# Kernel tuning notes

Measured on AMD Instinct MI355X. Metric: run time of the kernel, lower is better.

The kernel has to match this reference:

```python
import jax, jax.numpy as jnp
import numpy as np

B, N_IN, D_IN = 64, 2048, 16
N_OUT, D_OUT = 32, 32
ROUTINGS = 3
EPS = 1e-7


def squash(s, axis=-1):
    # standard CapsNet squash: s * ||s||^2 / (1 + ||s||^2) / ||s||
    sq_norm = jnp.sum(jnp.square(s), axis=axis, keepdims=True)
    scale = sq_norm / (1.0 + sq_norm) / jnp.sqrt(sq_norm + EPS)
    return s * scale


def setup_inputs() -> dict:
    key = jax.random.key(0)
    k1, k2 = jax.random.split(key)
    inputs = jax.random.normal(k1, (B, N_IN, D_IN), dtype=jnp.float32)
    # glorot-uniform-ish scale for [N_out, N_in, D_out, D_in] weight
    limit = np.sqrt(6.0 / (D_IN + D_OUT)).astype(np.float32)
    weight_matrix = jax.random.uniform(k2, (N_OUT, N_IN, D_OUT, D_IN), dtype=jnp.float32,
                                       minval=-limit, maxval=limit)
    return {"inputs": inputs, "weight_matrix": weight_matrix}


def reference(inputs, weight_matrix):
    # u_hat[b,o,i,d] = W[o,i,d,k] @ x[b,i,k]  (replaces tile + map_fn matmul)
    u_hat = jnp.einsum('oidk,bik->boid', weight_matrix, inputs)  # [B, N_out, N_in, D_out]
    b_logits = jnp.zeros((inputs.shape[0], N_OUT, 1, N_IN), dtype=u_hat.dtype)
    v = None
    for r in range(ROUTINGS):
        c = jax.nn.softmax(b_logits, axis=1)                      # softmax over output capsules
        s = jnp.einsum('boli,boid->bold', c, u_hat)               # [B, N_out, 1, D_out]
        v = squash(s)
        if r < ROUTINGS - 1:
            b_logits = b_logits + jnp.einsum('bold,boid->boli', v, u_hat)
    return jnp.squeeze(v, axis=2)                                 # [B, N_out, D_out]
```

## Files before the change

### kernel.cpp

```cpp
#include <hip/hip_runtime.h>

#define B_    64
#define NI    2048
#define DK    16
#define NO    32
#define DOUT  32
#define EPSQ  1e-7f

typedef unsigned u32x2 __attribute__((ext_vector_type(2)));
typedef unsigned u32x4 __attribute__((ext_vector_type(4)));

__device__ __forceinline__ unsigned pack2_bf16(float a, float b) {
    unsigned ua = __float_as_uint(a);
    unsigned ub = __float_as_uint(b);
    ua = (ua + 0x7fffu + ((ua >> 16) & 1u)) >> 16;
    ub = (ub + 0x7fffu + ((ub >> 16) & 1u)) >> 16;
    return ua | (ub << 16);
}
__device__ __forceinline__ float bf_lo(unsigned w) { return __uint_as_float(w << 16); }
__device__ __forceinline__ float bf_hi(unsigned w) { return __uint_as_float(w & 0xffff0000u); }


constexpr int WSTRIDE = 516;

__global__ __launch_bounds__(512)
void compute_uhat(const float* __restrict__ x, const float* __restrict__ W,
                  ushort* __restrict__ U)
{
    __shared__ float Ws[NO * WSTRIDE];
    __shared__ float xs[B_ * DK];
    const int i = blockIdx.x;
    const int t = threadIdx.x;

    if (t < 256) {
        const int b = t >> 2, k4 = t & 3;
        float4 v = *(const float4*)(x + ((size_t)b * NI + i) * DK + k4 * 4);
        *(float4*)&xs[b * DK + k4 * 4] = v;
    }

    #pragma unroll
    for (int jj = 0; jj < 8; ++jj) {
        const int p  = t + 512 * jj;
        const int oo = p >> 7;
        const int cc = p & 127;
        float4 v = ((const float4*)(W + ((size_t)oo * NI + i) * (DOUT * DK)))[cc];
        *(float4*)&Ws[oo * WSTRIDE + cc * 4] = v;
    }

    const int o  = t & 31;
    const int q  = (t >> 5) & 7;
    const int bh = t >> 8;

    __syncthreads();

    float w[64];
    {
        const float* wr = &Ws[o * WSTRIDE + q * 64];
        #pragma unroll
        for (int m = 0; m < 16; ++m) {
            float4 v = *(const float4*)(wr + 4 * m);
            w[4*m+0] = v.x; w[4*m+1] = v.y; w[4*m+2] = v.z; w[4*m+3] = v.w;
        }
    }

    const int j = q >> 1, half = q & 1;

    for (int bb = 0; bb < 32; ++bb) {
        const int b = bh * 32 + bb;
        const float4* xv = (const float4*)&xs[b * DK];
        const float4 x0 = xv[0], x1 = xv[1], x2 = xv[2], x3 = xv[3];

        float acc[4];
        #pragma unroll
        for (int dl = 0; dl < 4; ++dl) {
            const float* wr = &w[dl * 16];
            float a;
            a  = wr[0]  * x0.x + wr[1]  * x0.y + wr[2]  * x0.z + wr[3]  * x0.w;
            a += wr[4]  * x1.x + wr[5]  * x1.y + wr[6]  * x1.z + wr[7]  * x1.w;
            a += wr[8]  * x2.x + wr[9]  * x2.y + wr[10] * x2.z + wr[11] * x2.w;
            a += wr[12] * x3.x + wr[13] * x3.y + wr[14] * x3.z + wr[15] * x3.w;
            acc[dl] = a;
        }

        u32x2 pk;
        pk.x = pack2_bf16(acc[0], acc[1]);
        pk.y = pack2_bf16(acc[2], acc[3]);
        const size_t off = ((((size_t)b * NI + i) * 4 + j) * NO + o) * 8 + half * 4;
        __builtin_nontemporal_store(pk, (u32x2*)(U + off));
    }
}

constexpr int SU_SEG = 16;
constexpr int SU_IPB = NI / SU_SEG;

__global__ __launch_bounds__(256)
void sum_u(const ushort* __restrict__ U, float* __restrict__ s0)
{
    const int t    = threadIdx.x;
    const int b    = blockIdx.x >> 4;
    const int iseg = blockIdx.x & (SU_SEG - 1);
    const int c    = t & 127;
    const int half = t >> 7;

    float acc[8];
    #pragma unroll
    for (int k = 0; k < 8; ++k) acc[k] = 0.f;

    const u32x4* up = (const u32x4*)U
        + ((size_t)b * NI + (size_t)iseg * SU_IPB + half) * 128 + c;

    #pragma unroll 8
    for (int it = 0; it < SU_IPB / 2; ++it) {
        u32x4 w = __builtin_nontemporal_load(up);
        up += 256;
        acc[0] += bf_lo(w.x); acc[1] += bf_hi(w.x);
        acc[2] += bf_lo(w.y); acc[3] += bf_hi(w.y);
        acc[4] += bf_lo(w.z); acc[5] += bf_hi(w.z);
        acc[6] += bf_lo(w.w); acc[7] += bf_hi(w.w);
    }

    const int o = c & 31, j = c >> 5;
    float* sp = s0 + (size_t)b * (NO * DOUT) + o * DOUT + j * 8;
    #pragma unroll
    for (int k = 0; k < 8; ++k)
        atomicAdd(&sp[k], acc[k] * 0.03125f);
}

__device__ __forceinline__ void proc_one(const u32x4* cr, const float* vs, float* sacc)
{
    unsigned cw[16];
    #pragma unroll
    for (int jj = 0; jj < 4; ++jj) {
        cw[4*jj+0] = cr[jj].x; cw[4*jj+1] = cr[jj].y;
        cw[4*jj+2] = cr[jj].z; cw[4*jj+3] = cr[jj].w;
    }

    float l0 = 0.f, l1 = 0.f, l2 = 0.f, l3 = 0.f;
    #pragma unroll
    for (int m = 0; m < 16; m += 4) {
        const int d0 = (m >> 2) * 8;
        l0 = fmaf(vs[d0+0], bf_lo(cw[m+0]), l0);
        l0 = fmaf(vs[d0+1], bf_hi(cw[m+0]), l0);
        l1 = fmaf(vs[d0+2], bf_lo(cw[m+1]), l1);
        l1 = fmaf(vs[d0+3], bf_hi(cw[m+1]), l1);
        l2 = fmaf(vs[d0+4], bf_lo(cw[m+2]), l2);
        l2 = fmaf(vs[d0+5], bf_hi(cw[m+2]), l2);
        l3 = fmaf(vs[d0+6], bf_lo(cw[m+3]), l3);
        l3 = fmaf(vs[d0+7], bf_hi(cw[m+3]), l3);
    }
    const float logit = (l0 + l1) + (l2 + l3);

    float mx = logit;
    #pragma unroll
    for (int msk = 16; msk >= 1; msk >>= 1) mx = fmaxf(mx, __shfl_xor(mx, msk));
    const float e = __expf(logit - mx);
    float ssum = e;
    #pragma unroll
    for (int msk = 16; msk >= 1; msk >>= 1) ssum += __shfl_xor(ssum, msk);
    const float c = e / ssum;

    #pragma unroll
    for (int m = 0; m < 16; ++m) {
        const int d0 = (m >> 2) * 8 + (m & 3) * 2;
        sacc[d0]     = fmaf(c, bf_lo(cw[m]), sacc[d0]);
        sacc[d0 + 1] = fmaf(c, bf_hi(cw[m]), sacc[d0 + 1]);
    }
}

constexpr int BPB = 16;
constexpr int NIB = NI / BPB / 16;

template<int R>
__global__ __launch_bounds__(256)
void routing_mid(const ushort* __restrict__ U, const float* __restrict__ sA,
                 const float* __restrict__ sB, float* __restrict__ s_out)
{
    __shared__ float sblk[NO * DOUT];
    __shared__ float vsh[NO][DOUT + 1];
    const int t  = threadIdx.x;
    const int b  = blockIdx.x >> 4;
    const int i0 = (blockIdx.x & (BPB - 1)) * (NI / BPB);

    {
        const int oo = t >> 3;
        const int dg = t & 7;
        float4 sv = *(const float4*)(sA + ((size_t)b * NO + oo) * DOUT + dg * 4);
        float sq = sv.x*sv.x + sv.y*sv.y + sv.z*sv.z + sv.w*sv.w;
        #pragma unroll
        for (int msk = 4; msk >= 1; msk >>= 1) sq += __shfl_xor(sq, msk);
        float sc = sq / (1.f + sq) * rsqrtf(sq + EPSQ);
        float v0 = sv.x * sc, v1 = sv.y * sc, v2 = sv.z * sc, v3 = sv.w * sc;
        if (R == 2) {
            float4 s2v = *(const float4*)(sB + ((size_t)b * NO + oo) * DOUT + dg * 4);
            float sq2 = s2v.x*s2v.x + s2v.y*s2v.y + s2v.z*s2v.z + s2v.w*s2v.w;
            #pragma unroll
            for (int msk = 4; msk >= 1; msk >>= 1) sq2 += __shfl_xor(sq2, msk);
            float sc2 = sq2 / (1.f + sq2) * rsqrtf(sq2 + EPSQ);
            v0 += s2v.x * sc2; v1 += s2v.y * sc2; v2 += s2v.z * sc2; v3 += s2v.w * sc2;
        }
        vsh[oo][dg*4+0] = v0; vsh[oo][dg*4+1] = v1;
        vsh[oo][dg*4+2] = v2; vsh[oo][dg*4+3] = v3;
    }
    for (int n = t; n < NO * DOUT; n += 256) sblk[n] = 0.f;
    __syncthreads();

    const int o  = t & 31;
    const int hw = t >> 5;

    float vs[DOUT];
    #pragma unroll
    for (int d = 0; d < DOUT; ++d) vs[d] = vsh[o][d];

    float sacc[DOUT];
    #pragma unroll
    for (int d = 0; d < DOUT; ++d) sacc[d] = 0.f;

    const u32x4* up = (const u32x4*)U + ((size_t)b * NI + i0 + 2 * hw) * (4 * NO) + o;
    const size_t step = (size_t)16 * 4 * NO;

    u32x4 cur[8];
    #pragma unroll
    for (int jj = 0; jj < 4; ++jj) {
        cur[jj]     = __builtin_nontemporal_load(up + jj * NO);
        cur[4 + jj] = __builtin_nontemporal_load(up + 4 * NO + jj * NO);
    }
    up += step;

    for (int ii = 0; ii < NIB; ++ii) {
        u32x4 nxt[8];
        if (ii + 1 < NIB) {
            #pragma unroll
            for (int jj = 0; jj < 4; ++jj) {
                nxt[jj]     = __builtin_nontemporal_load(up + jj * NO);
                nxt[4 + jj] = __builtin_nontemporal_load(up + 4 * NO + jj * NO);
            }
            up += step;
        }

        proc_one(&cur[0], vs, sacc);
        proc_one(&cur[4], vs, sacc);

        #pragma unroll
        for (int jj = 0; jj < 8; ++jj) cur[jj] = nxt[jj];
    }

    #pragma unroll
    for (int d = 0; d < DOUT; ++d) sacc[d] += __shfl_xor(sacc[d], 32);

    if ((t & 32) == 0) {
        #pragma unroll
        for (int d = 0; d < DOUT; ++d)
            atomicAdd(&sblk[o * DOUT + ((d + o) & 31)], sacc[d]);
    }
    __syncthreads();

    float* sp = s_out + (size_t)b * NO * DOUT;
    for (int n = t; n < NO * DOUT; n += 256) {
        const int oo = n >> 5, ds = n & 31;
        const int dd = (ds - oo) & 31;
        atomicAdd(&sp[oo * DOUT + dd], sblk[n]);
    }
}

__global__ __launch_bounds__(256)
void squash_final(const float* __restrict__ s, float* __restrict__ out)
{
    const int tid  = threadIdx.x;
    const int pair = blockIdx.x * 8 + (tid >> 5);
    const int d    = tid & 31;
    const int idx  = pair * DOUT + d;

    const float val = s[idx];
    float sq = val * val;
    #pragma unroll
    for (int msk = 16; msk >= 1; msk >>= 1) sq += __shfl_xor(sq, msk);

    const float scale = sq / (1.f + sq) * rsqrtf(sq + EPSQ);
    out[idx] = val * scale;
}

__global__ __launch_bounds__(256)
void squash_update(const float* __restrict__ s, float* __restrict__ Vsum,
                   float* __restrict__ out, int last)
{
    const int tid  = threadIdx.x;
    const int pair = blockIdx.x * 8 + (tid >> 5);
    const int d    = tid & 31;
    const int idx  = pair * DOUT + d;

    const float val = s[idx];
    float sq = val * val;
    #pragma unroll
    for (int msk = 16; msk >= 1; msk >>= 1) sq += __shfl_xor(sq, msk);

    const float scale = sq / (1.f + sq) * rsqrtf(sq + EPSQ);
    const float v = val * scale;

    if (last) out[idx] = v;
    else      Vsum[idx] += v;
}

constexpr int BTILE  = 16;
constexpr int ITILE  = 32;
constexpr int CHUNKS = NI / ITILE;
constexpr int GB     = B_ / BTILE;
constexpr int WROW   = DOUT * DK + 4;

__global__ __launch_bounds__(512)
void routing_pass(const float* __restrict__ x, const float* __restrict__ W,
                  const float* __restrict__ Vsum, float* __restrict__ s_out)
{
    __shared__ float W_s[NO * WROW];
    const int tid   = threadIdx.x;
    const int o     = tid & 31;
    const int bl    = tid >> 5;
    const int chunk = blockIdx.x & (CHUNKS - 1);
    const int gb    = blockIdx.x / CHUNKS;
    const int b     = gb * BTILE + bl;

    float vs[DOUT];
    {
        const float4* vp = (const float4*)(Vsum + (size_t)(b * NO + o) * DOUT);
        #pragma unroll
        for (int qq = 0; qq < 8; ++qq) {
            float4 t2 = vp[qq];
            vs[4*qq+0] = t2.x; vs[4*qq+1] = t2.y; vs[4*qq+2] = t2.z; vs[4*qq+3] = t2.w;
        }
    }
    float sacc[DOUT];
    #pragma unroll
    for (int d = 0; d < DOUT; ++d) sacc[d] = 0.f;

    const int o_ld = tid >> 4;
    const int lpos = tid & 15;

    for (int ii = 0; ii < ITILE; ++ii) {
        const int i = chunk * ITILE + ii;
        __syncthreads();
        const float4* wsrc = (const float4*)W + ((size_t)o_ld * NI + i) * (DOUT * DK / 4);
        #pragma unroll
        for (int jj = 0; jj < 8; ++jj) {
            const int f4pos = lpos + 16 * jj;
            float4 v = wsrc[f4pos];
            *(float4*)&W_s[o_ld * WROW + f4pos * 4] = v;
        }
        __syncthreads();

        const float4* xg = (const float4*)(x + ((size_t)b * NI + i) * DK);
        const float4 xr0 = xg[0], xr1 = xg[1], xr2 = xg[2], xr3 = xg[3];

        float u[DOUT];
        float logit = 0.f;
        const float* wrow = &W_s[o * WROW];
        #pragma unroll
        for (int d = 0; d < DOUT; ++d) {
            const float4 w0 = *(const float4*)(wrow + d * DK + 0);
            const float4 w1 = *(const float4*)(wrow + d * DK + 4);
            const float4 w2 = *(const float4*)(wrow + d * DK + 8);
            const float4 w3 = *(const float4*)(wrow + d * DK + 12);
            float acc;
            acc  = w0.x * xr0.x + w0.y * xr0.y + w0.z * xr0.z + w0.w * xr0.w;
            acc += w1.x * xr1.x + w1.y * xr1.y + w1.z * xr1.z + w1.w * xr1.w;
            acc += w2.x * xr2.x + w2.y * xr2.y + w2.z * xr2.z + w2.w * xr2.w;
            acc += w3.x * xr3.x + w3.y * xr3.y + w3.z * xr3.z + w3.w * xr3.w;
            u[d]  = acc;
            logit = fmaf(vs[d], acc, logit);
        }

        float m = logit;
        #pragma unroll
        for (int msk = 16; msk >= 1; msk >>= 1) m = fmaxf(m, __shfl_xor(m, msk));
        const float e = __expf(logit - m);
        float ssum = e;
        #pragma unroll
        for (int msk = 16; msk >= 1; msk >>= 1) ssum += __shfl_xor(ssum, msk);
        const float c = e / ssum;

        #pragma unroll
        for (int d = 0; d < DOUT; ++d) sacc[d] = fmaf(c, u[d], sacc[d]);
    }

    float* sp = s_out + (size_t)(b * NO + o) * DOUT;
    #pragma unroll
    for (int d = 0; d < DOUT; ++d) atomicAdd(&sp[d], sacc[d]);
}

extern "C" void kernel_launch(void* const* d_in, const int* in_sizes, int n_in,
                              void* d_out, int out_size, void* d_ws, size_t ws_size,
                              hipStream_t stream)
{
    const float* x = (const float*)d_in[0];
    const float* W = (const float*)d_in[1];
    float* out = (float*)d_out;

    float* s0 = (float*)d_ws;
    float* s1 = s0 + (size_t)B_ * NO * DOUT;
    float* s2 = s1 + (size_t)B_ * NO * DOUT;
    ushort* U = (ushort*)((char*)d_ws + (1 << 20));

    const size_t need = (1 << 20) + (size_t)B_ * NI * NO * DOUT * sizeof(ushort);

    hipMemsetAsync(d_ws, 0, (size_t)3 * B_ * NO * DOUT * sizeof(float), stream);

    if (ws_size >= need) {
        compute_uhat<<<dim3(NI), dim3(512), 0, stream>>>(x, W, U);
        sum_u<<<dim3(B_ * SU_SEG), dim3(256), 0, stream>>>(U, s0);
        routing_mid<1><<<dim3(B_ * BPB), dim3(256), 0, stream>>>(U, s0, s0, s1);
        routing_mid<2><<<dim3(B_ * BPB), dim3(256), 0, stream>>>(U, s0, s1, s2);
        squash_final<<<dim3(B_ * NO / 8), dim3(256), 0, stream>>>(s2, out);
    } else {
        for (int r = 0; r < 3; ++r) {
            if (r > 0)
                hipMemsetAsync(s0, 0, (size_t)B_ * NO * DOUT * sizeof(float), stream);
            routing_pass<<<dim3(GB * CHUNKS), dim3(512), 0, stream>>>(x, W, s1, s0);
            squash_update<<<dim3(B_ * NO / 8), dim3(256), 0, stream>>>(s0, s1, out, r == 2);
        }
    }
}
```

Before: 470.9 us.

## Split u_hat blocks by output half, use per-segment partial sums instead of atomics

```diff
diff --git a/kernel.cpp b/kernel.cpp
--- a/kernel.cpp
+++ b/kernel.cpp
@@ -10,6 +10,8 @@
 typedef unsigned u32x2 __attribute__((ext_vector_type(2)));
 typedef unsigned u32x4 __attribute__((ext_vector_type(4)));
 
+constexpr int PSEG = 32;
+
 __device__ __forceinline__ unsigned pack2_bf16(float a, float b) {
     unsigned ua = __float_as_uint(a);
     unsigned ub = __float_as_uint(b);
@@ -21,16 +23,18 @@
 __device__ __forceinline__ float bf_hi(unsigned w) { return __uint_as_float(w & 0xffff0000u); }
 
 
-constexpr int WSTRIDE = 516;
-
-__global__ __launch_bounds__(512)
+constexpr int CU_STR = 516;
+
+__global__ __launch_bounds__(512, 8)
 void compute_uhat(const float* __restrict__ x, const float* __restrict__ W,
                   ushort* __restrict__ U)
 {
-    __shared__ float Ws[NO * WSTRIDE];
+    __shared__ float Ws[16 * CU_STR];
     __shared__ float xs[B_ * DK];
-    const int i = blockIdx.x;
-    const int t = threadIdx.x;
+    const int bx = blockIdx.x;
+    const int i  = bx >> 1;
+    const int oh = bx & 1;
+    const int t  = threadIdx.x;
 
     if (t < 256) {
         const int b = t >> 2, k4 = t & 3;
@@ -39,66 +43,74 @@
     }
 
     #pragma unroll
-    for (int jj = 0; jj < 8; ++jj) {
-        const int p  = t + 512 * jj;
+    for (int pp = 0; pp < 4; ++pp) {
+        const int p  = t + 512 * pp;
         const int oo = p >> 7;
         const int cc = p & 127;
-        float4 v = ((const float4*)(W + ((size_t)oo * NI + i) * (DOUT * DK)))[cc];
-        *(float4*)&Ws[oo * WSTRIDE + cc * 4] = v;
-    }
-
-    const int o  = t & 31;
-    const int q  = (t >> 5) & 7;
-    const int bh = t >> 8;
+        float4 v = ((const float4*)(W + ((size_t)(oh * 16 + oo) * NI + i) * (DOUT * DK)))[cc];
+        *(float4*)&Ws[oo * CU_STR + cc * 4] = v;
+    }
+
+    const int o2 = t & 15;
+    const int q  = (t >> 4) & 7;
+    const int bh = t >> 7;
 
     __syncthreads();
 
-    float w[64];
-    {
-        const float* wr = &Ws[o * WSTRIDE + q * 64];
-        #pragma unroll
-        for (int m = 0; m < 16; ++m) {
-            float4 v = *(const float4*)(wr + 4 * m);
-            w[4*m+0] = v.x; w[4*m+1] = v.y; w[4*m+2] = v.z; w[4*m+3] = v.w;
-        }
-    }
-
     const int j = q >> 1, half = q & 1;
-
-    for (int bb = 0; bb < 32; ++bb) {
-        const int b = bh * 32 + bb;
-        const float4* xv = (const float4*)&xs[b * DK];
-        const float4 x0 = xv[0], x1 = xv[1], x2 = xv[2], x3 = xv[3];
-
-        float acc[4];
-        #pragma unroll
-        for (int dl = 0; dl < 4; ++dl) {
-            const float* wr = &w[dl * 16];
-            float a;
-            a  = wr[0]  * x0.x + wr[1]  * x0.y + wr[2]  * x0.z + wr[3]  * x0.w;
-            a += wr[4]  * x1.x + wr[5]  * x1.y + wr[6]  * x1.z + wr[7]  * x1.w;
-            a += wr[8]  * x2.x + wr[9]  * x2.y + wr[10] * x2.z + wr[11] * x2.w;
-            a += wr[12] * x3.x + wr[13] * x3.y + wr[14] * x3.z + wr[15] * x3.w;
-            acc[dl] = a;
-        }
-
-        u32x2 pk;
-        pk.x = pack2_bf16(acc[0], acc[1]);
-        pk.y = pack2_bf16(acc[2], acc[3]);
-        const size_t off = ((((size_t)b * NI + i) * 4 + j) * NO + o) * 8 + half * 4;
-        __builtin_nontemporal_store(pk, (u32x2*)(U + off));
-    }
-}
-
-constexpr int SU_SEG = 16;
-constexpr int SU_IPB = NI / SU_SEG;
-
+    const int o = oh * 16 + o2;
+    const float* wrow = &Ws[o2 * CU_STR + q * 64];
+
+    #pragma unroll
+    for (int bg = 0; bg < 4; ++bg) {
+        const int b0 = bh * 16 + bg * 4;
+        float acc[4][4];
+        #pragma unroll
+        for (int bv = 0; bv < 4; ++bv)
+            #pragma unroll
+            for (int dl = 0; dl < 4; ++dl) acc[bv][dl] = 0.f;
+
+        #pragma unroll
+        for (int k4 = 0; k4 < 4; ++k4) {
+            float4 xr[4];
+            #pragma unroll
+            for (int bv = 0; bv < 4; ++bv)
+                xr[bv] = *(const float4*)&xs[(b0 + bv) * DK + k4 * 4];
+            #pragma unroll
+            for (int dl = 0; dl < 4; ++dl) {
+                const float4 w4 = *(const float4*)&wrow[16 * dl + 4 * k4];
+                #pragma unroll
+                for (int bv = 0; bv < 4; ++bv) {
+                    float a = acc[bv][dl];
+                    a = fmaf(w4.x, xr[bv].x, a);
+                    a = fmaf(w4.y, xr[bv].y, a);
+                    a = fmaf(w4.z, xr[bv].z, a);
+                    a = fmaf(w4.w, xr[bv].w, a);
+                    acc[bv][dl] = a;
+                }
+            }
+        }
+
+        #pragma unroll
+        for (int bv = 0; bv < 4; ++bv) {
+            const int b = b0 + bv;
+            u32x2 pk;
+            pk.x = pack2_bf16(acc[bv][0], acc[bv][1]);
+            pk.y = pack2_bf16(acc[bv][2], acc[bv][3]);
+            const size_t off = ((((size_t)b * NI + i) * 4 + j) * NO + o) * 8 + half * 4;
+            __builtin_nontemporal_store(pk, (u32x2*)(U + off));
+        }
+    }
+}
+
+template<bool PART>
 __global__ __launch_bounds__(256)
 void sum_u(const ushort* __restrict__ U, float* __restrict__ s0)
 {
+    __shared__ float red[128 * 9];
     const int t    = threadIdx.x;
-    const int b    = blockIdx.x >> 4;
-    const int iseg = blockIdx.x & (SU_SEG - 1);
+    const int b    = blockIdx.x >> 5;
+    const int iseg = blockIdx.x & 31;
     const int c    = t & 127;
     const int half = t >> 7;
 
@@ -107,10 +119,10 @@
     for (int k = 0; k < 8; ++k) acc[k] = 0.f;
 
     const u32x4* up = (const u32x4*)U
-        + ((size_t)b * NI + (size_t)iseg * SU_IPB + half) * 128 + c;
+        + ((size_t)b * NI + (size_t)iseg * (NI / PSEG) + half) * 128 + c;
 
     #pragma unroll 8
-    for (int it = 0; it < SU_IPB / 2; ++it) {
+    for (int it = 0; it < (NI / PSEG) / 2; ++it) {
         u32x4 w = __builtin_nontemporal_load(up);
         up += 256;
         acc[0] += bf_lo(w.x); acc[1] += bf_hi(w.x);
@@ -119,185 +131,186 @@
         acc[6] += bf_lo(w.w); acc[7] += bf_hi(w.w);
     }
 
-    const int o = c & 31, j = c >> 5;
-    float* sp = s0 + (size_t)b * (NO * DOUT) + o * DOUT + j * 8;
-    #pragma unroll
-    for (int k = 0; k < 8; ++k)
-        atomicAdd(&sp[k], acc[k] * 0.03125f);
-}
-
-__device__ __forceinline__ void proc_one(const u32x4* cr, const float* vs, float* sacc)
-{
-    unsigned cw[16];
-    #pragma unroll
-    for (int jj = 0; jj < 4; ++jj) {
-        cw[4*jj+0] = cr[jj].x; cw[4*jj+1] = cr[jj].y;
-        cw[4*jj+2] = cr[jj].z; cw[4*jj+3] = cr[jj].w;
-    }
-
-    float l0 = 0.f, l1 = 0.f, l2 = 0.f, l3 = 0.f;
-    #pragma unroll
-    for (int m = 0; m < 16; m += 4) {
-        const int d0 = (m >> 2) * 8;
-        l0 = fmaf(vs[d0+0], bf_lo(cw[m+0]), l0);
-        l0 = fmaf(vs[d0+1], bf_hi(cw[m+0]), l0);
-        l1 = fmaf(vs[d0+2], bf_lo(cw[m+1]), l1);
-        l1 = fmaf(vs[d0+3], bf_hi(cw[m+1]), l1);
-        l2 = fmaf(vs[d0+4], bf_lo(cw[m+2]), l2);
-        l2 = fmaf(vs[d0+5], bf_hi(cw[m+2]), l2);
-        l3 = fmaf(vs[d0+6], bf_lo(cw[m+3]), l3);
-        l3 = fmaf(vs[d0+7], bf_hi(cw[m+3]), l3);
-    }
-    const float logit = (l0 + l1) + (l2 + l3);
-
-    float mx = logit;
-    #pragma unroll
-    for (int msk = 16; msk >= 1; msk >>= 1) mx = fmaxf(mx, __shfl_xor(mx, msk));
-    const float e = __expf(logit - mx);
-    float ssum = e;
-    #pragma unroll
-    for (int msk = 16; msk >= 1; msk >>= 1) ssum += __shfl_xor(ssum, msk);
-    const float c = e / ssum;
-
-    #pragma unroll
-    for (int m = 0; m < 16; ++m) {
-        const int d0 = (m >> 2) * 8 + (m & 3) * 2;
-        sacc[d0]     = fmaf(c, bf_lo(cw[m]), sacc[d0]);
-        sacc[d0 + 1] = fmaf(c, bf_hi(cw[m]), sacc[d0 + 1]);
-    }
-}
-
-constexpr int BPB = 16;
-constexpr int NIB = NI / BPB / 16;
-
-template<int R>
-__global__ __launch_bounds__(256)
+    if (half == 1) {
+        #pragma unroll
+        for (int k = 0; k < 8; ++k) red[c * 9 + k] = acc[k];
+    }
+    __syncthreads();
+    if (half == 0) {
+        #pragma unroll
+        for (int k = 0; k < 8; ++k) acc[k] = (acc[k] + red[c * 9 + k]) * 0.03125f;
+
+        const int o = c & 31, j = c >> 5;
+        if (PART) {
+            float* sp = s0 + ((size_t)(b * PSEG + iseg)) * 1024 + o * 32 + j * 8;
+            float4 lo = {acc[0], acc[1], acc[2], acc[3]};
+            float4 hi = {acc[4], acc[5], acc[6], acc[7]};
+            *(float4*)sp = lo;
+            *(float4*)(sp + 4) = hi;
+        } else {
+            float* sp = s0 + (size_t)b * 1024 + o * 32 + j * 8;
+            #pragma unroll
+            for (int k = 0; k < 8; ++k) atomicAdd(&sp[k], acc[k]);
+        }
+    }
+}
+
+template<int R, bool PART>
+__global__ __launch_bounds__(256, 5)
 void routing_mid(const ushort* __restrict__ U, const float* __restrict__ sA,
                  const float* __restrict__ sB, float* __restrict__ s_out)
 {
     __shared__ float sblk[NO * DOUT];
     __shared__ float vsh[NO][DOUT + 1];
-    const int t  = threadIdx.x;
-    const int b  = blockIdx.x >> 4;
-    const int i0 = (blockIdx.x & (BPB - 1)) * (NI / BPB);
+    const int t    = threadIdx.x;
+    const int b    = blockIdx.x >> 5;
+    const int iseg = blockIdx.x & 31;
+    const int i0   = iseg * (NI / PSEG);
 
     {
         const int oo = t >> 3;
         const int dg = t & 7;
-        float4 sv = *(const float4*)(sA + ((size_t)b * NO + oo) * DOUT + dg * 4);
+        float4 sv;
+        if (PART) {
+            float4 a = {0.f, 0.f, 0.f, 0.f};
+            for (int is = 0; is < PSEG; ++is) {
+                float4 p = *(const float4*)(sA + ((size_t)(b * PSEG + is)) * 1024 + oo * 32 + dg * 4);
+                a.x += p.x; a.y += p.y; a.z += p.z; a.w += p.w;
+            }
+            sv = a;
+        } else {
+            sv = *(const float4*)(sA + (size_t)b * 1024 + oo * 32 + dg * 4);
+        }
         float sq = sv.x*sv.x + sv.y*sv.y + sv.z*sv.z + sv.w*sv.w;
         #pragma unroll
         for (int msk = 4; msk >= 1; msk >>= 1) sq += __shfl_xor(sq, msk);
         float sc = sq / (1.f + sq) * rsqrtf(sq + EPSQ);
         float v0 = sv.x * sc, v1 = sv.y * sc, v2 = sv.z * sc, v3 = sv.w * sc;
         if (R == 2) {
-            float4 s2v = *(const float4*)(sB + ((size_t)b * NO + oo) * DOUT + dg * 4);
+            float4 s2v;
+            if (PART) {
+                float4 a = {0.f, 0.f, 0.f, 0.f};
+                for (int is = 0; is < PSEG; ++is) {
+                    float4 p = *(const float4*)(sB + ((size_t)(b * PSEG + is)) * 1024 + oo * 32 + dg * 4);
+                    a.x += p.x; a.y += p.y; a.z += p.z; a.w += p.w;
+                }
+                s2v = a;
+            } else {
+                s2v = *(const float4*)(sB + (size_t)b * 1024 + oo * 32 + dg * 4);
+            }
             float sq2 = s2v.x*s2v.x + s2v.y*s2v.y + s2v.z*s2v.z + s2v.w*s2v.w;
             #pragma unroll
             for (int msk = 4; msk >= 1; msk >>= 1) sq2 += __shfl_xor(sq2, msk);
             float sc2 = sq2 / (1.f + sq2) * rsqrtf(sq2 + EPSQ);
             v0 += s2v.x * sc2; v1 += s2v.y * sc2; v2 += s2v.z * sc2; v3 += s2v.w * sc2;
         }
-        vsh[oo][dg*4+0] = v0; vsh[oo][dg*4+1] = v1;
-        vsh[oo][dg*4+2] = v2; vsh[oo][dg*4+3] = v3;
+        vsh[oo][dg * 4 + 0] = v0; vsh[oo][dg * 4 + 1] = v1;
+        vsh[oo][dg * 4 + 2] = v2; vsh[oo][dg * 4 + 3] = v3;
     }
     for (int n = t; n < NO * DOUT; n += 256) sblk[n] = 0.f;
     __syncthreads();
 
-    const int o  = t & 31;
-    const int hw = t >> 5;
-
-    float vs[DOUT];
-    #pragma unroll
-    for (int d = 0; d < DOUT; ++d) vs[d] = vsh[o][d];
-
-    float sacc[DOUT];
-    #pragma unroll
-    for (int d = 0; d < DOUT; ++d) sacc[d] = 0.f;
-
-    const u32x4* up = (const u32x4*)U + ((size_t)b * NI + i0 + 2 * hw) * (4 * NO) + o;
-    const size_t step = (size_t)16 * 4 * NO;
-
-    u32x4 cur[8];
-    #pragma unroll
-    for (int jj = 0; jj < 4; ++jj) {
-        cur[jj]     = __builtin_nontemporal_load(up + jj * NO);
-        cur[4 + jj] = __builtin_nontemporal_load(up + 4 * NO + jj * NO);
-    }
-    up += step;
-
-    for (int ii = 0; ii < NIB; ++ii) {
-        u32x4 nxt[8];
-        if (ii + 1 < NIB) {
-            #pragma unroll
-            for (int jj = 0; jj < 4; ++jj) {
-                nxt[jj]     = __builtin_nontemporal_load(up + jj * NO);
-                nxt[4 + jj] = __builtin_nontemporal_load(up + 4 * NO + jj * NO);
-            }
-            up += step;
-        }
-
-        proc_one(&cur[0], vs, sacc);
-        proc_one(&cur[4], vs, sacc);
-
-        #pragma unroll
-        for (int jj = 0; jj < 8; ++jj) cur[jj] = nxt[jj];
-    }
-
-    #pragma unroll
-    for (int d = 0; d < DOUT; ++d) sacc[d] += __shfl_xor(sacc[d], 32);
-
-    if ((t & 32) == 0) {
-        #pragma unroll
-        for (int d = 0; d < DOUT; ++d)
-            atomicAdd(&sblk[o * DOUT + ((d + o) & 31)], sacc[d]);
+    const int lane = t & 63;
+    const int o    = lane & 31;
+    const int dh   = lane >> 5;
+    const int wv   = t >> 6;
+
+    float vs[16];
+    #pragma unroll
+    for (int ld = 0; ld < 16; ++ld) vs[ld] = vsh[o][dh * 16 + ld];
+
+    float sacc[16];
+    #pragma unroll
+    for (int ld = 0; ld < 16; ++ld) sacc[ld] = 0.f;
+
+    const u32x4* up = (const u32x4*)U
+        + (((size_t)b * NI + i0 + wv * 16) * 4 + 2 * dh) * NO + o;
+
+    u32x4 c0 = __builtin_nontemporal_load(up);
+    u32x4 c1 = __builtin_nontemporal_load(up + NO);
+    up += 4 * NO;
+
+    for (int ii = 0; ii < 16; ++ii) {
+        u32x4 n0 = {}, n1 = {};
+        const bool more = (ii < 15);
+        if (more) {
+            n0 = __builtin_nontemporal_load(up);
+            n1 = __builtin_nontemporal_load(up + NO);
+            up += 4 * NO;
+        }
+
+        float lp = 0.f;
+        #pragma unroll
+        for (int wi = 0; wi < 4; ++wi) {
+            lp = fmaf(vs[2*wi],     bf_lo(c0[wi]), lp);
+            lp = fmaf(vs[2*wi + 1], bf_hi(c0[wi]), lp);
+            lp = fmaf(vs[8 + 2*wi],     bf_lo(c1[wi]), lp);
+            lp = fmaf(vs[8 + 2*wi + 1], bf_hi(c1[wi]), lp);
+        }
+        lp += __shfl_xor(lp, 32);
+
+        float mx = lp;
+        #pragma unroll
+        for (int msk = 16; msk >= 1; msk >>= 1) mx = fmaxf(mx, __shfl_xor(mx, msk));
+        const float e = __expf(lp - mx);
+        float ss = e;
+        #pragma unroll
+        for (int msk = 16; msk >= 1; msk >>= 1) ss += __shfl_xor(ss, msk);
+        const float cc = e / ss;
+
+        #pragma unroll
+        for (int wi = 0; wi < 4; ++wi) {
+            sacc[2*wi]     = fmaf(cc, bf_lo(c0[wi]), sacc[2*wi]);
+            sacc[2*wi + 1] = fmaf(cc, bf_hi(c0[wi]), sacc[2*wi + 1]);
+            sacc[8 + 2*wi]     = fmaf(cc, bf_lo(c1[wi]), sacc[8 + 2*wi]);
+            sacc[8 + 2*wi + 1] = fmaf(cc, bf_hi(c1[wi]), sacc[8 + 2*wi + 1]);
+        }
+
+        if (more) { c0 = n0; c1 = n1; }
+    }
+
+    #pragma unroll
+    for (int ld = 0; ld < 16; ++ld) {
+        const int d = dh * 16 + ld;
+        atomicAdd(&sblk[o * 32 + ((d + o) & 31)], sacc[ld]);
     }
     __syncthreads();
 
-    float* sp = s_out + (size_t)b * NO * DOUT;
-    for (int n = t; n < NO * DOUT; n += 256) {
-        const int oo = n >> 5, ds = n & 31;
-        const int dd = (ds - oo) & 31;
-        atomicAdd(&sp[oo * DOUT + dd], sblk[n]);
-    }
-}
-
+    if (PART) {
+        float* sp = s_out + ((size_t)(b * PSEG + iseg)) * 1024;
+        for (int n = t; n < NO * DOUT; n += 256) {
+            const int oo = n >> 5, dd = n & 31;
+            sp[n] = sblk[oo * 32 + ((dd + oo) & 31)];
+        }
+    } else {
+        float* sp = s_out + (size_t)b * 1024;
+        for (int n = t; n < NO * DOUT; n += 256) {
+            const int oo = n >> 5, dd = n & 31;
+            atomicAdd(&sp[n], sblk[oo * 32 + ((dd + oo) & 31)]);
+        }
+    }
+}
+
+template<bool PART>
 __global__ __launch_bounds__(256)
 void squash_final(const float* __restrict__ s, float* __restrict__ out)
 {
-    const int tid  = threadIdx.x;
-    const int pair = blockIdx.x * 8 + (tid >> 5);
-    const int d    = tid & 31;
-    const int idx  = pair * DOUT + d;
-
-    const float val = s[idx];
+    const int g = blockIdx.x * 256 + threadIdx.x;
+    float val;
+    if (PART) {
+        const int b = g >> 10, slot = g & 1023;
+        float a = 0.f;
+        for (int is = 0; is < PSEG; ++is)
+            a += s[((size_t)(b * PSEG + is)) * 1024 + slot];
+        val = a;
+    } else {
+        val = s[g];
+    }
     float sq = val * val;
     #pragma unroll
     for (int msk = 16; msk >= 1; msk >>= 1) sq += __shfl_xor(sq, msk);
-
     const float scale = sq / (1.f + sq) * rsqrtf(sq + EPSQ);
-    out[idx] = val * scale;
-}
-
-__global__ __launch_bounds__(256)
-void squash_update(const float* __restrict__ s, float* __restrict__ Vsum,
-                   float* __restrict__ out, int last)
-{
-    const int tid  = threadIdx.x;
-    const int pair = blockIdx.x * 8 + (tid >> 5);
-    const int d    = tid & 31;
-    const int idx  = pair * DOUT + d;
-
-    const float val = s[idx];
-    float sq = val * val;
-    #pragma unroll
-    for (int msk = 16; msk >= 1; msk >>= 1) sq += __shfl_xor(sq, msk);
-
-    const float scale = sq / (1.f + sq) * rsqrtf(sq + EPSQ);
-    const float v = val * scale;
-
-    if (last) out[idx] = v;
-    else      Vsum[idx] += v;
+    out[g] = val * scale;
 }
 
 constexpr int BTILE  = 16;
@@ -385,6 +398,27 @@
     for (int d = 0; d < DOUT; ++d) atomicAdd(&sp[d], sacc[d]);
 }
 
+__global__ __launch_bounds__(256)
+void squash_update(const float* __restrict__ s, float* __restrict__ Vsum,
+                   float* __restrict__ out, int last)
+{
+    const int tid  = threadIdx.x;
+    const int pair = blockIdx.x * 8 + (tid >> 5);
+    const int d    = tid & 31;
+    const int idx  = pair * DOUT + d;
+
+    const float val = s[idx];
+    float sq = val * val;
+    #pragma unroll
+    for (int msk = 16; msk >= 1; msk >>= 1) sq += __shfl_xor(sq, msk);
+
+    const float scale = sq / (1.f + sq) * rsqrtf(sq + EPSQ);
+    const float v = val * scale;
+
+    if (last) out[idx] = v;
+    else      Vsum[idx] += v;
+}
+
 extern "C" void kernel_launch(void* const* d_in, const int* in_sizes, int n_in,
                               void* d_out, int out_size, void* d_ws, size_t ws_size,
                               hipStream_t stream)
@@ -393,25 +427,42 @@
     const float* W = (const float*)d_in[1];
     float* out = (float*)d_out;
 
-    float* s0 = (float*)d_ws;
-    float* s1 = s0 + (size_t)B_ * NO * DOUT;
-    float* s2 = s1 + (size_t)B_ * NO * DOUT;
-    ushort* U = (ushort*)((char*)d_ws + (1 << 20));
-
-    const size_t need = (1 << 20) + (size_t)B_ * NI * NO * DOUT * sizeof(ushort);
-
-    hipMemsetAsync(d_ws, 0, (size_t)3 * B_ * NO * DOUT * sizeof(float), stream);
-
-    if (ws_size >= need) {
-        compute_uhat<<<dim3(NI), dim3(512), 0, stream>>>(x, W, U);
-        sum_u<<<dim3(B_ * SU_SEG), dim3(256), 0, stream>>>(U, s0);
-        routing_mid<1><<<dim3(B_ * BPB), dim3(256), 0, stream>>>(U, s0, s0, s1);
-        routing_mid<2><<<dim3(B_ * BPB), dim3(256), 0, stream>>>(U, s0, s1, s2);
-        squash_final<<<dim3(B_ * NO / 8), dim3(256), 0, stream>>>(s2, out);
+    const size_t UBYTES = (size_t)B_ * NI * NO * DOUT * sizeof(ushort);
+    const size_t PBY    = (size_t)B_ * PSEG * 1024 * sizeof(float);
+
+    const size_t need_part   = 3 * PBY + UBYTES;
+    const size_t need_atomic = (1 << 20) + UBYTES;
+
+    if (ws_size >= need_part) {
+        float* P0 = (float*)d_ws;
+        float* P1 = (float*)((char*)d_ws + PBY);
+        float* P2 = (float*)((char*)d_ws + 2 * PBY);
+        ushort* U = (ushort*)((char*)d_ws + 3 * PBY);
+
+        compute_uhat<<<dim3(NI * 2), dim3(512), 0, stream>>>(x, W, U);
+        sum_u<true><<<dim3(B_ * PSEG), dim3(256), 0, stream>>>(U, P0);
+        routing_mid<1, true><<<dim3(B_ * PSEG), dim3(256), 0, stream>>>(U, P0, P0, P1);
+        routing_mid<2, true><<<dim3(B_ * PSEG), dim3(256), 0, stream>>>(U, P0, P1, P2);
+        squash_final<true><<<dim3(B_ * NO * DOUT / 256), dim3(256), 0, stream>>>(P2, out);
+    } else if (ws_size >= need_atomic) {
+        float* s0 = (float*)d_ws;
+        float* s1 = s0 + (size_t)B_ * 1024;
+        float* s2 = s1 + (size_t)B_ * 1024;
+        ushort* U = (ushort*)((char*)d_ws + (1 << 20));
+
+        hipMemsetAsync(d_ws, 0, (size_t)3 * B_ * 1024 * sizeof(float), stream);
+        compute_uhat<<<dim3(NI * 2), dim3(512), 0, stream>>>(x, W, U);
+        sum_u<false><<<dim3(B_ * PSEG), dim3(256), 0, stream>>>(U, s0);
+        routing_mid<1, false><<<dim3(B_ * PSEG), dim3(256), 0, stream>>>(U, s0, s0, s1);
+        routing_mid<2, false><<<dim3(B_ * PSEG), dim3(256), 0, stream>>>(U, s0, s1, s2);
+        squash_final<false><<<dim3(B_ * NO * DOUT / 256), dim3(256), 0, stream>>>(s2, out);
     } else {
+        float* s0 = (float*)d_ws;
+        float* s1 = s0 + (size_t)B_ * 1024;
+        hipMemsetAsync(d_ws, 0, (size_t)2 * B_ * 1024 * sizeof(float), stream);
         for (int r = 0; r < 3; ++r) {
             if (r > 0)
-                hipMemsetAsync(s0, 0, (size_t)B_ * NO * DOUT * sizeof(float), stream);
+                hipMemsetAsync(s0, 0, (size_t)B_ * 1024 * sizeof(float), stream);
             routing_pass<<<dim3(GB * CHUNKS), dim3(512), 0, stream>>>(x, W, s1, s0);
             squash_update<<<dim3(B_ * NO / 8), dim3(256), 0, stream>>>(s0, s1, out, r == 2);
         }
```

Measured after the change: 1.492 ms. 3.17x slower.
